# Kernel tuning notes

Hardware: AMD Instinct MI355X
Metric: run time of the kernel (lower is better)

The kernel has to match this reference:

```python
import jax, jax.numpy as jnp
import numpy as np

N = 50000        # nodes
E = 800_000      # edges (avg degree 16)
D_IN, D_HID, D_OUT = 512, 512, 256
P_DROP = 0.5


def setup_inputs() -> dict:
    key = jax.random.key(0)
    k0, k1, k2, k3 = jax.random.split(key, 4)
    x = jax.random.normal(k0, (N, D_IN), dtype=jnp.float32)
    edge_index = jax.random.randint(k1, (2, E), 0, N, dtype=jnp.int64)
    W1 = jax.random.normal(k2, (D_HID, D_IN), dtype=jnp.float32) * 0.02
    b1 = jnp.zeros((D_HID,), dtype=jnp.float32)
    W2 = jax.random.normal(k3, (D_OUT, D_HID), dtype=jnp.float32) * 0.02
    b2 = jnp.zeros((D_OUT,), dtype=jnp.float32)
    return {"x": x, "edge_index": edge_index, "W1": W1, "b1": b1, "W2": W2, "b2": b2}


def _gcn_norm(edge_index, n):
    # add self loops, then symmetric GCN normalization: D^-1/2 (A+I) D^-1/2
    src, dst = edge_index[0], edge_index[1]
    loops = jnp.arange(n, dtype=src.dtype)
    src = jnp.concatenate([src, loops])
    dst = jnp.concatenate([dst, loops])
    deg = jax.ops.segment_sum(jnp.ones_like(src, dtype=jnp.float32), dst, num_segments=n)
    dinv = jax.lax.rsqrt(deg)  # deg >= 1 because of self loops
    norm = dinv[src] * dinv[dst]  # [E+N]
    return src, dst, norm


def _propagate(x, src, dst, norm):
    # out[i] = sum_{(j->i)} norm_e * x[j]
    return jax.ops.segment_sum(x[src] * norm[:, None], dst, num_segments=x.shape[0])


def reference(x, edge_index, W1, b1, W2, b2):
    src, dst, norm = _gcn_norm(edge_index, x.shape[0])
    # SGConv layer 1 (K=1): propagate then linear
    h = _propagate(x, src, dst, norm) @ W1.T + b1
    h = jax.nn.relu(h)
    # F.dropout(p) with training=True default -> deterministic fixed-key mask here
    keep = jax.random.bernoulli(jax.random.key(42), 1.0 - P_DROP, h.shape)
    embedding = jnp.where(keep, h / (1.0 - P_DROP), 0.0)
    # SGConv layer 2
    out = _propagate(embedding, src, dst, norm) @ W2.T + b2
    return embedding, out
```

## Files before the change

kernel.cpp:

```cpp
#include <hip/hip_runtime.h>

typedef unsigned short u16t;
typedef __attribute__((ext_vector_type(8))) short short8;
typedef __attribute__((ext_vector_type(4))) short short4v;
typedef __attribute__((ext_vector_type(4))) float f32x4;
typedef __attribute__((ext_vector_type(2))) float f32x2;
typedef __attribute__((ext_vector_type(4))) unsigned short u16x4;
typedef __attribute__((ext_vector_type(4))) unsigned int u32x4;
typedef __attribute__((ext_vector_type(2))) unsigned int u32x2;
typedef __attribute__((ext_vector_type(4))) int i32x4;

__device__ __forceinline__ float bf2f(short b) {
  return __uint_as_float(((unsigned)(unsigned short)b) << 16);
}
__device__ __forceinline__ u16t f2bf(float f) {
  unsigned u = __float_as_uint(f);
  u += 0x7FFFu + ((u >> 16) & 1u);
  return (u16t)(u >> 16);
}

__device__ __forceinline__ bool keep_mask(unsigned flat) {
  const unsigned k0 = 0u, k1 = 42u;
  const unsigned k2 = k0 ^ k1 ^ 0x1BD11BDAu;
  unsigned x0 = 0u + k0;
  unsigned x1 = flat + k1;
#define TF_R(r) { x0 += x1; x1 = (x1 << r) | (x1 >> (32 - r)); x1 ^= x0; }
  TF_R(13) TF_R(15) TF_R(26) TF_R(6)  x0 += k1; x1 += k2 + 1u;
  TF_R(17) TF_R(29) TF_R(16) TF_R(24) x0 += k2; x1 += k0 + 2u;
  TF_R(13) TF_R(15) TF_R(26) TF_R(6)  x0 += k0; x1 += k1 + 3u;
  TF_R(17) TF_R(29) TF_R(16) TF_R(24) x0 += k1; x1 += k2 + 4u;
  TF_R(13) TF_R(15) TF_R(26) TF_R(6)  x0 += k2; x1 += k0 + 5u;
#undef TF_R
  return ((x0 ^ x1) >> 31) == 0u;
}

__device__ __forceinline__ void load_lds16(const u16t* g, u16t* l) {
  __builtin_amdgcn_global_load_lds((__attribute__((address_space(1))) void*)g,
                                   (__attribute__((address_space(3))) void*)l,
                                   16, 0, 0);
}

__global__ void cvt_bf16(const float* __restrict__ s, u16t* __restrict__ d, int n) {
  int i = (blockIdx.x * 256 + threadIdx.x) * 4;
  if (i < n) {
    f32x4 v = *(const f32x4*)&s[i];
    u16x4 o = { f2bf(v.x), f2bf(v.y), f2bf(v.z), f2bf(v.w) };
    *(u16x4*)&d[i] = o;
  }
}

__global__ __launch_bounds__(256) void mask_kernel(unsigned* __restrict__ mask, int nn) {
  const int node = blockIdx.x * 256 + threadIdx.x;
  const int sl = blockIdx.y;
  if (node >= nn) return;
  unsigned base = ((unsigned)node * 16u + (unsigned)sl) * 32u;
  unsigned m = 0u;
  for (int k = 0; k < 32; ++k) m |= (keep_mask(base + (unsigned)k) ? 1u : 0u) << k;
  mask[(size_t)sl * nn + node] = m;
}

__global__ void count_edges(const int* __restrict__ dst, int E, int* __restrict__ cnt) {
  int e = blockIdx.x * 256 + threadIdx.x;
  if (e < E) atomicAdd(&cnt[dst[e]], 1);
}

__global__ __launch_bounds__(256) void bin_hist(const int* __restrict__ cnt,
                                                int* __restrict__ hist, int n) {
  __shared__ int sh[16];
  const int tid = threadIdx.x;
  if (tid < 16) sh[tid] = 0;
  __syncthreads();
  int i = blockIdx.x * 256 + tid;
  if (i < n) {
    int b = (cnt[i] + 8) >> 3;
    atomicAdd(&sh[b < 15 ? b : 15], 1);
  }
  __syncthreads();
  if (tid < 16 && sh[tid] > 0) atomicAdd(&hist[tid], sh[tid]);
}

__global__ void bin_scan(const int* __restrict__ hist, int* __restrict__ binCursor) {
  if (threadIdx.x == 0 && blockIdx.x == 0) {
    int s = 0;
    for (int b = 15; b >= 0; --b) { binCursor[b] = s; s += hist[b]; }
  }
}

__global__ __launch_bounds__(256) void rowp_build(const int* __restrict__ cnt,
    i32x4* __restrict__ ndr, int* __restrict__ cursor, float* __restrict__ dinv,
    int* __restrict__ gctr, u16t* __restrict__ colu,
    int* __restrict__ binCursor, u16t* __restrict__ perm, int n) {
  __shared__ int sd[256];
  __shared__ int sbase;
  __shared__ int shist[16];
  __shared__ int sbinbase[16];
  const int tid = threadIdx.x;
  const int i = blockIdx.x * 256 + tid;
  int c = (i < n) ? cnt[i] : 0;
  int cs = c + 1;
  int p = (i < n) ? ((cs + 7) & ~7) : 0;
  int v = p;
  sd[tid] = v;
  if (tid < 16) shist[tid] = 0;
  __syncthreads();
  for (int o = 1; o < 256; o <<= 1) {
    int t2 = (tid >= o) ? sd[tid - o] : 0;
    __syncthreads();
    v += t2;
    sd[tid] = v;
    __syncthreads();
  }
  int b = p >> 3;
  b = b < 15 ? b : 15;
  int rank = 0;
  if (i < n) rank = atomicAdd(&shist[b], 1);
  if (tid == 255) sbase = atomicAdd(gctr, v);
  __syncthreads();
  if (tid < 16) sbinbase[tid] = (shist[tid] > 0) ? atomicAdd(&binCursor[tid], shist[tid]) : 0;
  __syncthreads();
  if (i < n) {
    int start = sbase + v - p;
    cursor[i] = start;
    float dv = rsqrtf((float)cs);
    dinv[i] = dv;
    i32x4 r;
    r[0] = start; r[1] = start + p; r[2] = __float_as_int(dv); r[3] = 0;
    ndr[i] = r;
    colu[start + c] = (u16t)i;
    for (int q = c + 1; q < p; ++q) colu[start + q] = (u16t)n;
    perm[sbinbase[b] + rank] = (u16t)i;
  }
}

__global__ void fill_csr(const int* __restrict__ src, const int* __restrict__ dst, int E,
                         int* __restrict__ cursor, u16t* __restrict__ col) {
  int e = blockIdx.x * 256 + threadIdx.x;
  if (e < E) {
    int d = dst[e];
    int pos = atomicAdd(&cursor[d], 1);
    col[pos] = (u16t)src[e];
  }
}

__global__ __launch_bounds__(256) void gemm_bt_sl(const u16t* __restrict__ A,
                                                  const u16t* __restrict__ B,
                                                  u16t* __restrict__ C,
                                                  int K, int Mrows,
                                                  const float* __restrict__ dinv,
                                                  int Nclamp) {
  __shared__ __align__(16) u16t lA[128 * 32];
  __shared__ __align__(16) u16t lB[128 * 32];
  const int tid = threadIdx.x;
  const int wave = tid >> 6, lane = tid & 63;
  const int wm = (wave & 1) * 64, wn = (wave >> 1) * 64;
  const int lrow = lane & 15, lq = lane >> 4;
  const u16t* Ab = A + (size_t)blockIdx.x * 128 * K;
  const u16t* Bb = B + (size_t)blockIdx.y * 128 * K;
  const int r0 = tid >> 2, c0 = (tid & 3) * 8;
  const int ldsOff = __builtin_amdgcn_readfirstlane((tid >> 6) * 512);

  f32x4 acc[4][4];
  const f32x4 zero = {0.f, 0.f, 0.f, 0.f};
#pragma unroll
  for (int mi = 0; mi < 4; ++mi)
#pragma unroll
    for (int ni = 0; ni < 4; ++ni) acc[mi][ni] = zero;

  for (int kt = 0; kt < K; kt += 32) {
    __syncthreads();
    load_lds16(Ab + (size_t)r0 * K + kt + c0, &lA[ldsOff]);
    load_lds16(Ab + (size_t)(r0 + 64) * K + kt + c0, &lA[2048 + ldsOff]);
    load_lds16(Bb + (size_t)r0 * K + kt + c0, &lB[ldsOff]);
    load_lds16(Bb + (size_t)(r0 + 64) * K + kt + c0, &lB[2048 + ldsOff]);
    __syncthreads();
    short8 af[4], bfr[4];
#pragma unroll
    for (int mi = 0; mi < 4; ++mi)
      af[mi] = *(const short8*)&lA[(wm + mi * 16 + lrow) * 32 + lq * 8];
#pragma unroll
    for (int ni = 0; ni < 4; ++ni)
      bfr[ni] = *(const short8*)&lB[(wn + ni * 16 + lrow) * 32 + lq * 8];
#pragma unroll
    for (int mi = 0; mi < 4; ++mi)
#pragma unroll
      for (int ni = 0; ni < 4; ++ni)
        acc[mi][ni] = __builtin_amdgcn_mfma_f32_16x16x32_bf16(af[mi], bfr[ni], acc[mi][ni], 0, 0, 0);
  }

  const int crow0 = blockIdx.x * 128 + wm + lq * 4;
  const int ccol0 = blockIdx.y * 128 + wn + lrow;
#pragma unroll
  for (int mi = 0; mi < 4; ++mi)
#pragma unroll
    for (int r = 0; r < 4; ++r) {
      const int row = crow0 + mi * 16 + r;
      const float dr = (row < Nclamp) ? dinv[row] : 0.f;
#pragma unroll
      for (int ni = 0; ni < 4; ++ni) {
        int cc = ccol0 + ni * 16;
        size_t idx = ((size_t)(cc >> 5) * Mrows + row) * 32 + (cc & 31);
        C[idx] = f2bf(dr * acc[mi][ni][r]);
      }
    }
}

__device__ __forceinline__ void gather8w(const char* __restrict__ Tb, u32x4 cw,
                                         unsigned flb, f32x2 acc[4]) {
  unsigned off[8];
#pragma unroll
  for (int q = 0; q < 4; ++q) {
    off[2 * q]     = ((cw[q] & 0xFFFFu) << 6) | flb;
    off[2 * q + 1] = ((cw[q] >> 16) << 6) | flb;
  }
  u32x4 w[8];
#pragma unroll
  for (int q = 0; q < 8; ++q) w[q] = *(const u32x4*)(Tb + (size_t)off[q]);
#pragma unroll
  for (int q = 0; q < 8; ++q)
#pragma unroll
    for (int d = 0; d < 4; ++d) {
      f32x2 v = { __uint_as_float(w[q][d] << 16),
                  __uint_as_float(w[q][d] & 0xFFFF0000u) };
      acc[d] += v;
    }
}

__global__ __launch_bounds__(256) void prop1_kernel(const u16t* __restrict__ T0,
    const u16t* __restrict__ colu, const i32x4* __restrict__ ndr,
    const u16t* __restrict__ perm, const float* __restrict__ b1,
    const unsigned* __restrict__ kmask,
    float* __restrict__ embf, u16t* __restrict__ embb, int n, int Mrows, int chunks) {
  const int t = threadIdx.x;
  const unsigned flb = (unsigned)(t & 3) * 16u;
  const int fl8 = (t & 3) * 8;
  const int bid = blockIdx.x;
  const int half = chunks << 3;
  const int phase = bid >= half;
  const int rem = bid - (phase ? half : 0);
  const int sl = (rem & 7) + (phase << 3);
  const int slot = (rem >> 3) * 64 + (t >> 2);
  if (slot >= n) return;
  const int i = (int)perm[slot];

  const char* Tb = (const char*)T0 + (size_t)sl * ((size_t)Mrows * 64);
  const i32x4 nd = ndr[i];
  const float di = __int_as_float(nd[2]);
  f32x2 a[4] = {{0.f, 0.f}, {0.f, 0.f}, {0.f, 0.f}, {0.f, 0.f}};

  int e = nd[0];
  const int end = nd[1];
  u32x4 cw = *(const u32x4*)&colu[e];
  e += 8;
  while (e < end) {
    u32x4 nw = *(const u32x4*)&colu[e];
    e += 8;
    gather8w(Tb, cw, flb, a);
    cw = nw;
  }
  gather8w(Tb, cw, flb, a);

  const int f = sl * 32 + fl8;
  const unsigned km = kmask[(size_t)sl * n + i] >> fl8;
  float acc[8] = {a[0].x, a[0].y, a[1].x, a[1].y, a[2].x, a[2].y, a[3].x, a[3].y};
  f32x4 o0, o1;
  short8 ob;
#pragma unroll
  for (int j = 0; j < 8; ++j) {
    float h = di * acc[j] + b1[f + j];
    h = fmaxf(h, 0.f);
    float eb = ((km >> j) & 1u) ? 2.f * h : 0.f;
    if (j < 4) o0[j] = eb; else o1[j - 4] = eb;
    ob[j] = (short)f2bf(eb);
  }
  __builtin_nontemporal_store(o0, (f32x4*)&embf[(size_t)i * 512 + f]);
  __builtin_nontemporal_store(o1, (f32x4*)&embf[(size_t)i * 512 + f + 4]);
  __builtin_nontemporal_store(ob, (short8*)&embb[(size_t)i * 512 + f]);
}

__global__ __launch_bounds__(256) void prop2_kernel(const u16t* __restrict__ T0,
    const u16t* __restrict__ colu, const i32x4* __restrict__ ndr,
    const u16t* __restrict__ perm, const float* __restrict__ b2,
    float* __restrict__ outp, int n, int Mrows) {
  const int t = threadIdx.x;
  const unsigned flb = (unsigned)(t & 3) * 16u;
  const int fl8 = (t & 3) * 8;
  const int bid = blockIdx.x;
  const int sl = bid & 7;
  const int slot = (bid >> 3) * 64 + (t >> 2);
  if (slot >= n) return;
  const int i = (int)perm[slot];

  const char* Tb = (const char*)T0 + (size_t)sl * ((size_t)Mrows * 64);
  const i32x4 nd = ndr[i];
  const float di = __int_as_float(nd[2]);
  f32x2 a[4] = {{0.f, 0.f}, {0.f, 0.f}, {0.f, 0.f}, {0.f, 0.f}};

  int e = nd[0];
  const int end = nd[1];
  u32x4 cw = *(const u32x4*)&colu[e];
  e += 8;
  while (e < end) {
    u32x4 nw = *(const u32x4*)&colu[e];
    e += 8;
    gather8w(Tb, cw, flb, a);
    cw = nw;
  }
  gather8w(Tb, cw, flb, a);

  const int f = sl * 32 + fl8;
  float acc[8] = {a[0].x, a[0].y, a[1].x, a[1].y, a[2].x, a[2].y, a[3].x, a[3].y};
  f32x4 o0, o1;
#pragma unroll
  for (int j = 0; j < 8; ++j) {
    float v = di * acc[j] + b2[f + j];
    if (j < 4) o0[j] = v; else o1[j - 4] = v;
  }
  __builtin_nontemporal_store(o0, (f32x4*)&outp[(size_t)i * 256 + f]);
  __builtin_nontemporal_store(o1, (f32x4*)&outp[(size_t)i * 256 + f + 4]);
}

extern "C" void kernel_launch(void* const* d_in, const int* in_sizes, int n_in,
                              void* d_out, int out_size, void* d_ws, size_t ws_size,
                              hipStream_t stream) {
  (void)n_in; (void)out_size; (void)ws_size;
  const float* x  = (const float*)d_in[0];
  const int*   ei = (const int*)d_in[1];
  const float* W1 = (const float*)d_in[2];
  const float* b1 = (const float*)d_in[3];
  const float* W2 = (const float*)d_in[4];
  const float* b2 = (const float*)d_in[5];

  const int Nn = in_sizes[0] / 512;
  const int E  = in_sizes[1] / 2;
  const int Mpad = ((Nn + 127) / 128) * 128;
  const int K = 512;
  const int CH = (Nn + 63) / 64;

  char* ws = (char*)d_ws;
  size_t off = 0;
  auto take = [&](size_t bytes) -> char* {
    char* p = ws + off;
    off += (bytes + 255) & ~(size_t)255;
    return p;
  };
  u16t* xb   = (u16t*)take((size_t)Mpad * 512 * 2);
  u16t* y1s  = (u16t*)take((size_t)16 * Mpad * 32 * 2);
  u16t* W1b  = (u16t*)take((size_t)512 * 512 * 2);
  u16t* W2b  = (u16t*)take((size_t)256 * 512 * 2);
  int*   cnt    = (int*)take((size_t)(Nn + 33) * 4);
  int*   cursor = (int*)take((size_t)Nn * 4);
  float* dinv   = (float*)take((size_t)Nn * 4);
  i32x4* ndr    = (i32x4*)take((size_t)Nn * 16);
  u16t*  perm   = (u16t*)take((size_t)Nn * 2);
  u16t*  colu   = (u16t*)take((size_t)(E + 8 * (Nn + 1) + 64) * 2);
  unsigned* kmask = (unsigned*)take((size_t)Nn * 16 * 4);

  float* embf = (float*)d_out;
  float* outf = (float*)d_out + (size_t)Nn * 512;

  int* gctr      = cnt + Nn;
  int* hist      = cnt + Nn + 1;
  int* binCursor = cnt + Nn + 17;

  hipMemsetAsync(cnt, 0, (size_t)(Nn + 33) * 4, stream);

  const int n1 = Nn * 512;
  cvt_bf16<<<(n1 / 4 + 255) / 256, 256, 0, stream>>>(x, xb, n1);
  cvt_bf16<<<(512 * 512 / 4 + 255) / 256, 256, 0, stream>>>(W1, W1b, 512 * 512);
  cvt_bf16<<<(256 * 512 / 4 + 255) / 256, 256, 0, stream>>>(W2, W2b, 256 * 512);
  mask_kernel<<<dim3((Nn + 255) / 256, 16), 256, 0, stream>>>(kmask, Nn);

  count_edges<<<(E + 255) / 256, 256, 0, stream>>>(ei + E, E, cnt);
  bin_hist<<<(Nn + 255) / 256, 256, 0, stream>>>(cnt, hist, Nn);
  bin_scan<<<1, 64, 0, stream>>>(hist, binCursor);
  rowp_build<<<(Nn + 255) / 256, 256, 0, stream>>>(cnt, ndr, cursor, dinv, gctr,
                                                   colu, binCursor, perm, Nn);
  fill_csr<<<(E + 255) / 256, 256, 0, stream>>>(ei, ei + E, E, cursor, colu);

  dim3 g1(Mpad / 128, 4);
  gemm_bt_sl<<<g1, 256, 0, stream>>>(xb, W1b, y1s, K, Mpad, dinv, Nn);
  prop1_kernel<<<16 * CH, 256, 0, stream>>>(y1s, colu, ndr, perm, b1, kmask,
                                            embf, xb , Nn, Mpad, CH);

  u16t* zs = y1s;
  dim3 g2(Mpad / 128, 2);
  gemm_bt_sl<<<g2, 256, 0, stream>>>(xb, W2b, zs, K, Mpad, dinv, Nn);
  prop2_kernel<<<8 * CH, 256, 0, stream>>>(zs, colu, ndr, perm, b2, outf, Nn, Mpad);
}
```

Measured before the change: 592.6 us.

## Double-buffer gathers in propagation kernels and fuse mask generation into x conversion

The propagation kernels now keep two register buffers of eight gathered neighbour rows, so the loads for the next group of edges are issued before the current group is accumulated. This gives each thread more memory loads in flight to hide gather latency, at the cost of more vector registers and possibly lower occupancy. Separately, the dropout mask computation is merged into the fp32-to-bf16 conversion kernel for x, which removes one launch. The mask threads now use a flat indexing that keeps the same bit layout.

```diff
diff --git a/kernel.cpp b/kernel.cpp
--- a/kernel.cpp
+++ b/kernel.cpp
@@ -49,14 +49,21 @@
   }
 }
 
-__global__ __launch_bounds__(256) void mask_kernel(unsigned* __restrict__ mask, int nn) {
-  const int node = blockIdx.x * 256 + threadIdx.x;
-  const int sl = blockIdx.y;
-  if (node >= nn) return;
-  unsigned base = ((unsigned)node * 16u + (unsigned)sl) * 32u;
-  unsigned m = 0u;
-  for (int k = 0; k < 32; ++k) m |= (keep_mask(base + (unsigned)k) ? 1u : 0u) << k;
-  mask[(size_t)sl * nn + node] = m;
+__global__ __launch_bounds__(256) void cvt_x_mask(const float* __restrict__ s,
+    u16t* __restrict__ d, unsigned* __restrict__ mask, int n, int nn) {
+  int t = blockIdx.x * 256 + threadIdx.x;
+  int i = t * 4;
+  if (i < n) {
+    f32x4 v = *(const f32x4*)&s[i];
+    u16x4 o = { f2bf(v.x), f2bf(v.y), f2bf(v.z), f2bf(v.w) };
+    *(u16x4*)&d[i] = o;
+  }
+  if (t < nn * 16) {
+    unsigned base = (unsigned)t * 32u;
+    unsigned m = 0u;
+    for (int k = 0; k < 32; ++k) m |= (keep_mask(base + (unsigned)k) ? 1u : 0u) << k;
+    mask[(size_t)(t & 15) * nn + (t >> 4)] = m;
+  }
 }
 
 __global__ void count_edges(const int* __restrict__ dst, int E, int* __restrict__ cnt) {
@@ -204,17 +211,19 @@
     }
 }
 
-__device__ __forceinline__ void gather8w(const char* __restrict__ Tb, u32x4 cw,
-                                         unsigned flb, f32x2 acc[4]) {
+__device__ __forceinline__ void load8(const char* __restrict__ Tb, u32x4 cw,
+                                      unsigned flb, u32x4 w[8]) {
   unsigned off[8];
 #pragma unroll
   for (int q = 0; q < 4; ++q) {
     off[2 * q]     = ((cw[q] & 0xFFFFu) << 6) | flb;
     off[2 * q + 1] = ((cw[q] >> 16) << 6) | flb;
   }
-  u32x4 w[8];
 #pragma unroll
   for (int q = 0; q < 8; ++q) w[q] = *(const u32x4*)(Tb + (size_t)off[q]);
+}
+
+__device__ __forceinline__ void accum8(const u32x4 w[8], f32x2 acc[4]) {
 #pragma unroll
   for (int q = 0; q < 8; ++q)
 #pragma unroll
@@ -249,15 +258,37 @@
 
   int e = nd[0];
   const int end = nd[1];
-  u32x4 cw = *(const u32x4*)&colu[e];
+  u32x4 w0[8], w1[8];
+  {
+    u32x4 cw = *(const u32x4*)&colu[e];
+    load8(Tb, cw, flb, w0);
+  }
   e += 8;
-  while (e < end) {
-    u32x4 nw = *(const u32x4*)&colu[e];
+  if (e >= end) {
+    accum8(w0, a);
+  } else {
+    {
+      u32x4 cw = *(const u32x4*)&colu[e];
+      load8(Tb, cw, flb, w1);
+    }
     e += 8;
-    gather8w(Tb, cw, flb, a);
-    cw = nw;
-  }
-  gather8w(Tb, cw, flb, a);
+    for (;;) {
+      accum8(w0, a);
+      if (e >= end) { accum8(w1, a); break; }
+      {
+        u32x4 cw = *(const u32x4*)&colu[e];
+        load8(Tb, cw, flb, w0);
+      }
+      e += 8;
+      accum8(w1, a);
+      if (e >= end) { accum8(w0, a); break; }
+      {
+        u32x4 cw = *(const u32x4*)&colu[e];
+        load8(Tb, cw, flb, w1);
+      }
+      e += 8;
+    }
+  }
 
   const int f = sl * 32 + fl8;
   const unsigned km = kmask[(size_t)sl * n + i] >> fl8;
@@ -297,15 +328,37 @@
 
   int e = nd[0];
   const int end = nd[1];
-  u32x4 cw = *(const u32x4*)&colu[e];
+  u32x4 w0[8], w1[8];
+  {
+    u32x4 cw = *(const u32x4*)&colu[e];
+    load8(Tb, cw, flb, w0);
+  }
   e += 8;
-  while (e < end) {
-    u32x4 nw = *(const u32x4*)&colu[e];
+  if (e >= end) {
+    accum8(w0, a);
+  } else {
+    {
+      u32x4 cw = *(const u32x4*)&colu[e];
+      load8(Tb, cw, flb, w1);
+    }
     e += 8;
-    gather8w(Tb, cw, flb, a);
-    cw = nw;
-  }
-  gather8w(Tb, cw, flb, a);
+    for (;;) {
+      accum8(w0, a);
+      if (e >= end) { accum8(w1, a); break; }
+      {
+        u32x4 cw = *(const u32x4*)&colu[e];
+        load8(Tb, cw, flb, w0);
+      }
+      e += 8;
+      accum8(w1, a);
+      if (e >= end) { accum8(w0, a); break; }
+      {
+        u32x4 cw = *(const u32x4*)&colu[e];
+        load8(Tb, cw, flb, w1);
+      }
+      e += 8;
+    }
+  }
 
   const int f = sl * 32 + fl8;
   float acc[8] = {a[0].x, a[0].y, a[1].x, a[1].y, a[2].x, a[2].y, a[3].x, a[3].y};
@@ -365,10 +418,9 @@
   hipMemsetAsync(cnt, 0, (size_t)(Nn + 33) * 4, stream);
 
   const int n1 = Nn * 512;
-  cvt_bf16<<<(n1 / 4 + 255) / 256, 256, 0, stream>>>(x, xb, n1);
+  cvt_x_mask<<<(n1 / 4 + 255) / 256, 256, 0, stream>>>(x, xb, kmask, n1, Nn);
   cvt_bf16<<<(512 * 512 / 4 + 255) / 256, 256, 0, stream>>>(W1, W1b, 512 * 512);
   cvt_bf16<<<(256 * 512 / 4 + 255) / 256, 256, 0, stream>>>(W2, W2b, 256 * 512);
-  mask_kernel<<<dim3((Nn + 255) / 256, 16), 256, 0, stream>>>(kmask, Nn);
 
   count_edges<<<(E + 255) / 256, 256, 0, stream>>>(ei + E, E, cnt);
   bin_hist<<<(Nn + 255) / 256, 256, 0, stream>>>(cnt, hist, Nn);
```

Measured after the change: 583.6 us. About the same (-1.5%).
